# Kernel tuning notes

Hardware: AMD Instinct MI355X
Metric: run time of the kernel (lower is better)

The kernel has to match this reference:

```python
import jax, jax.numpy as jnp
import numpy as np

EPS = 1e-5  # torch LayerNorm default
B, S, D, H = 1, 2048, 512, 32
DH = D // H
DFF = 2 * D


def _ln(x, g, b):
    m = jnp.mean(x, -1, keepdims=True)
    v = jnp.var(x, -1, keepdims=True)
    return (x - m) * jax.lax.rsqrt(v + EPS) * g + b


def setup_inputs() -> dict:
    key = jax.random.key(0)
    ks = iter(jax.random.split(key, 24))
    sc = 1.0 / np.sqrt(D)

    def lin(k, din, dout):  # weight stored [in, out]; y = x @ W + b
        return jax.random.normal(k, (din, dout), jnp.float32) * (1.0 / np.sqrt(din))

    inp = {
        "x": jax.random.normal(next(ks), (B, S, D), jnp.float32),
        # outer pre-norm
        "ln0_g": jnp.ones((D,), jnp.float32), "ln0_b": jnp.zeros((D,), jnp.float32),
        # MultiHead per-branch LayerNorms (3 distinct param sets)
        "lnq_g": jnp.ones((D,), jnp.float32), "lnq_b": jnp.zeros((D,), jnp.float32),
        "lnk_g": jnp.ones((D,), jnp.float32), "lnk_b": jnp.zeros((D,), jnp.float32),
        "lnv_g": jnp.ones((D,), jnp.float32), "lnv_b": jnp.zeros((D,), jnp.float32),
        # QKV + output projections
        "Wq": lin(next(ks), D, D), "bq": jax.random.normal(next(ks), (D,), jnp.float32) * sc,
        "Wk": lin(next(ks), D, D), "bk": jax.random.normal(next(ks), (D,), jnp.float32) * sc,
        "Wv": lin(next(ks), D, D), "bv": jax.random.normal(next(ks), (D,), jnp.float32) * sc,
        "Wo": lin(next(ks), D, D), "bo": jax.random.normal(next(ks), (D,), jnp.float32) * sc,
        # FFN
        "lnf_g": jnp.ones((D,), jnp.float32), "lnf_b": jnp.zeros((D,), jnp.float32),
        "W1": lin(next(ks), D, DFF), "b1": jax.random.normal(next(ks), (DFF,), jnp.float32) * sc,
        "W2": lin(next(ks), DFF, D), "b2": jax.random.normal(next(ks), (D,), jnp.float32) * (1.0 / np.sqrt(DFF)),
    }
    return inp


def reference(x, ln0_g, ln0_b, lnq_g, lnq_b, lnk_g, lnk_b, lnv_g, lnv_b,
              Wq, bq, Wk, bk, Wv, bv, Wo, bo, lnf_g, lnf_b, W1, b1, W2, b2):
    # Encoder: x = norm(x); out = MHA(x,x,x) + x; x = out + FFN(out)
    xn = _ln(x, ln0_g, ln0_b)

    # --- MultiHead (dropout = identity, eval mode) ---
    q = _ln(xn, lnq_g, lnq_b) @ Wq + bq
    k = _ln(xn, lnk_g, lnk_b) @ Wk + bk
    v = _ln(xn, lnv_g, lnv_b) @ Wv + bv
    # [B,S,D] -> [B,H,S,DH]
    q = q.reshape(B, S, H, DH).transpose(0, 2, 1, 3)
    k = k.reshape(B, S, H, DH).transpose(0, 2, 1, 3)
    v = v.reshape(B, S, H, DH).transpose(0, 2, 1, 3)

    scores = jnp.einsum("bhqd,bhkd->bhqk", q, k) / (DH ** 0.5)
    causal = jnp.tril(jnp.ones((S, S), bool))  # make_mask: triu(k=1)==0
    scores = jnp.where(causal, scores, jnp.float32(-1e9))
    attn = jax.nn.softmax(scores, axis=-1)
    ctx = jnp.einsum("bhqk,bhkd->bhqd", attn, v)
    ctx = ctx.transpose(0, 2, 1, 3).reshape(B, S, D)
    mha = ctx @ Wo + bo

    out = mha + xn  # first residual

    # --- FFN branch: LN -> Linear(2D) -> ReLU -> Linear(D) -> ReLU ---
    h = jax.nn.relu(_ln(out, lnf_g, lnf_b) @ W1 + b1)
    ffn = jax.nn.relu(h @ W2 + b2)
    return out + ffn
```

## Files before the change

### kernel.cpp

```cpp
#include <hip/hip_runtime.h>

#define S 2048
#define D 512
#define NH 32
#define DHD 16
#define DFF 1024
#define EPS 1e-5f
#define C1 0.36067376022224085f

typedef unsigned short u16;
typedef __attribute__((ext_vector_type(8))) short short8;
typedef __attribute__((ext_vector_type(4))) float f32x4;
typedef __attribute__((ext_vector_type(16))) float f32x16;
typedef __attribute__((ext_vector_type(4))) unsigned short us4;

#define GL_LDS(gsrc, ldst)                                                   \
  __builtin_amdgcn_global_load_lds(                                          \
      (const __attribute__((address_space(1))) unsigned int*)(gsrc),         \
      (__attribute__((address_space(3))) unsigned int*)(ldst), 16, 0, 0)

static __device__ __forceinline__ u16 f2bf(float f) {
  union { float f; unsigned int i; } c; c.f = f;
  unsigned int x = c.i;
  return (u16)((x + 0x7fffu + ((x >> 16) & 1u)) >> 16);
}
static __device__ __forceinline__ float bf2f(u16 v) {
  union { unsigned int i; float f; } c; c.i = ((unsigned int)v) << 16;
  return c.f;
}

static __device__ __forceinline__ float tmax16(const float* p) {
  float a0 = fmaxf(p[0], p[1]), a1 = fmaxf(p[2], p[3]);
  float a2 = fmaxf(p[4], p[5]), a3 = fmaxf(p[6], p[7]);
  float a4 = fmaxf(p[8], p[9]), a5 = fmaxf(p[10], p[11]);
  float a6 = fmaxf(p[12], p[13]), a7 = fmaxf(p[14], p[15]);
  float b0 = fmaxf(a0, a1), b1 = fmaxf(a2, a3);
  float b2 = fmaxf(a4, a5), b3 = fmaxf(a6, a7);
  return fmaxf(fmaxf(b0, b1), fmaxf(b2, b3));
}
static __device__ __forceinline__ float tsum16(const float* p) {
  float a0 = p[0] + p[1], a1 = p[2] + p[3], a2 = p[4] + p[5], a3 = p[6] + p[7];
  float a4 = p[8] + p[9], a5 = p[10] + p[11], a6 = p[12] + p[13], a7 = p[14] + p[15];
  float b0 = a0 + a1, b1 = a2 + a3, b2 = a4 + a5, b3 = a6 + a7;
  return (b0 + b1) + (b2 + b3);
}

static __device__ __forceinline__ void block_reduce2(float& a, float& b, float* sm, int t) {
#pragma unroll
  for (int m = 1; m <= 32; m <<= 1) {
    a += __shfl_xor(a, m);
    b += __shfl_xor(b, m);
  }
  int w = t >> 6;
  if ((t & 63) == 0) { sm[w] = a; sm[4 + w] = b; }
  __syncthreads();
  a = sm[0] + sm[1] + sm[2] + sm[3];
  b = sm[4] + sm[5] + sm[6] + sm[7];
  __syncthreads();
}

__global__ __launch_bounds__(256) void ln0_kernel(
    const float* __restrict__ x,
    const float* __restrict__ g0, const float* __restrict__ b0,
    const float* __restrict__ gq, const float* __restrict__ bq,
    const float* __restrict__ gk, const float* __restrict__ bk,
    const float* __restrict__ gv, const float* __restrict__ bv,
    float* __restrict__ xn, u16* __restrict__ qin, u16* __restrict__ kin,
    u16* __restrict__ vin) {
  __shared__ float red[8];
  int row = blockIdx.x, t = threadIdx.x;
  const float* xr = x + (size_t)row * D;
  float a0 = xr[t], a1 = xr[t + 256];
  float s = a0 + a1, ss = a0 * a0 + a1 * a1;
  block_reduce2(s, ss, red, t);
  float mean = s * (1.0f / D);
  float var = ss * (1.0f / D) - mean * mean;
  float rs = rsqrtf(var + EPS);
  float y0 = (a0 - mean) * rs * g0[t] + b0[t];
  float y1 = (a1 - mean) * rs * g0[t + 256] + b0[t + 256];
  size_t o = (size_t)row * D + t;
  xn[o] = y0;
  xn[o + 256] = y1;
  float s2 = y0 + y1, ss2 = y0 * y0 + y1 * y1;
  block_reduce2(s2, ss2, red, t);
  float m2 = s2 * (1.0f / D);
  float v2 = ss2 * (1.0f / D) - m2 * m2;
  float rs2 = rsqrtf(v2 + EPS);
  float c0 = (y0 - m2) * rs2, c1 = (y1 - m2) * rs2;
  qin[o] = f2bf(c0 * gq[t] + bq[t]);
  qin[o + 256] = f2bf(c1 * gq[t + 256] + bq[t + 256]);
  kin[o] = f2bf(c0 * gk[t] + bk[t]);
  kin[o + 256] = f2bf(c1 * gk[t + 256] + bk[t + 256]);
  vin[o] = f2bf(c0 * gv[t] + bv[t]);
  vin[o + 256] = f2bf(c1 * gv[t + 256] + bv[t + 256]);
}

__global__ __launch_bounds__(256) void ln2_kernel(
    const float* __restrict__ in, const float* __restrict__ g,
    const float* __restrict__ b, u16* __restrict__ out) {
  __shared__ float red[8];
  int row = blockIdx.x, t = threadIdx.x;
  const float* xr = in + (size_t)row * D;
  float a0 = xr[t], a1 = xr[t + 256];
  float s = a0 + a1, ss = a0 * a0 + a1 * a1;
  block_reduce2(s, ss, red, t);
  float mean = s * (1.0f / D);
  float var = ss * (1.0f / D) - mean * mean;
  float rs = rsqrtf(var + EPS);
  size_t o = (size_t)row * D + t;
  out[o] = f2bf((a0 - mean) * rs * g[t] + b[t]);
  out[o + 256] = f2bf((a1 - mean) * rs * g[t + 256] + b[t + 256]);
}

static __device__ __forceinline__ void transpose_core(const float* __restrict__ W,
                                                      u16* __restrict__ Wt, int K, int N,
                                                      float (*tile)[33]) {
  int n0 = blockIdx.x * 32, k0 = blockIdx.y * 32;
  int tx = threadIdx.x, ty = threadIdx.y;
#pragma unroll
  for (int i = 0; i < 4; ++i)
    tile[ty + 8 * i][tx] = W[(size_t)(k0 + ty + 8 * i) * N + n0 + tx];
  __syncthreads();
#pragma unroll
  for (int i = 0; i < 4; ++i)
    Wt[(size_t)(n0 + ty + 8 * i) * K + k0 + tx] = f2bf(tile[tx][ty + 8 * i]);
}

__global__ void transpose4(const float* __restrict__ W0, const float* __restrict__ W1,
                           const float* __restrict__ W2, const float* __restrict__ W3,
                           u16* __restrict__ T0, u16* __restrict__ T1,
                           u16* __restrict__ T2, u16* __restrict__ T3) {
  __shared__ float tile[32][33];
  int z = blockIdx.z;
  const float* W = z == 0 ? W0 : z == 1 ? W1 : z == 2 ? W2 : W3;
  u16* T = z == 0 ? T0 : z == 1 ? T1 : z == 2 ? T2 : T3;
  transpose_core(W, T, D, D, tile);
}

__global__ void transpose_bf16(const float* __restrict__ W, u16* __restrict__ Wt,
                               int K, int N) {
  __shared__ float tile[32][33];
  transpose_core(W, Wt, K, N, tile);
}

static __device__ __forceinline__ void gemm_stage(
    const u16* __restrict__ A, const u16* __restrict__ Bt, int K,
    int m0, int n0, int kk, u16* As, u16* Bs, int w, int lane) {
  int r8 = lane >> 3;
  int c8 = ((lane & 7) ^ r8) * 8;
#pragma unroll
  for (int j = 0; j < 4; ++j) {
    int chunk = j * 4 + w;
    GL_LDS(A + (size_t)(m0 + chunk * 8 + r8) * K + kk + c8, As + chunk * 512);
  }
#pragma unroll
  for (int j = 0; j < 2; ++j) {
    int chunk = j * 4 + w;
    GL_LDS(Bt + (size_t)(n0 + chunk * 8 + r8) * K + kk + c8, Bs + chunk * 512);
  }
}

static __device__ __forceinline__ void gemm_acc128(
    const u16* __restrict__ A, const u16* __restrict__ Bt, int K, int m0, int n0,
    u16 (*As)[8192], u16 (*Bs)[4096], f32x4 acc[4][2]) {
  int t = threadIdx.x, w = t >> 6, lane = t & 63;
  int wm = w >> 1, wn = w & 1;
  int l16 = lane & 15, g4 = lane >> 4;
  gemm_stage(A, Bt, K, m0, n0, 0, As[0], Bs[0], w, lane);
  __syncthreads();
  int pb = 0;
  for (int kk = 0; kk < K; kk += 64) {
    if (kk + 64 < K)
      gemm_stage(A, Bt, K, m0, n0, kk + 64, As[pb ^ 1], Bs[pb ^ 1], w, lane);
#pragma unroll
    for (int ks = 0; ks < 2; ++ks) {
      short8 af[4], bf[2];
#pragma unroll
      for (int mi = 0; mi < 4; ++mi) {
        int row = wm * 64 + mi * 16 + l16;
        af[mi] = *(const short8*)&As[pb][row * 64 + (((ks * 4 + g4) ^ (l16 & 7)) * 8)];
      }
#pragma unroll
      for (int ni = 0; ni < 2; ++ni) {
        int row = wn * 32 + ni * 16 + l16;
        bf[ni] = *(const short8*)&Bs[pb][row * 64 + (((ks * 4 + g4) ^ (l16 & 7)) * 8)];
      }
#pragma unroll
      for (int mi = 0; mi < 4; ++mi)
#pragma unroll
        for (int ni = 0; ni < 2; ++ni)
          acc[mi][ni] = __builtin_amdgcn_mfma_f32_16x16x32_bf16(
              af[mi], bf[ni], acc[mi][ni], 0, 0, 0);
    }
    __syncthreads();
    pb ^= 1;
  }
}

template <bool RELU, bool RESID, bool OUTBF>
__global__ __launch_bounds__(256) void gemm_kernel(
    const u16* __restrict__ A, const u16* __restrict__ Bt,
    const float* __restrict__ bias, const float* __restrict__ resid,
    float* __restrict__ outf, u16* __restrict__ outb, int N, int K) {
  __shared__ u16 As[2][8192];
  __shared__ u16 Bs[2][4096];
  int m0 = blockIdx.x * 128, n0 = blockIdx.y * 64;
  f32x4 acc[4][2] = {};
  gemm_acc128(A, Bt, K, m0, n0, As, Bs, acc);
  int t = threadIdx.x, w = t >> 6, lane = t & 63;
  int wm = w >> 1, wn = w & 1;
  int l16 = lane & 15, g4 = lane >> 4;
#pragma unroll
  for (int mi = 0; mi < 4; ++mi)
#pragma unroll
    for (int ni = 0; ni < 2; ++ni)
#pragma unroll
      for (int r = 0; r < 4; ++r) {
        int row = m0 + wm * 64 + mi * 16 + g4 * 4 + r;
        int col = n0 + wn * 32 + ni * 16 + l16;
        float v = acc[mi][ni][r] + bias[col];
        if (RELU) v = fmaxf(v, 0.0f);
        if (RESID) v += resid[(size_t)row * N + col];
        if (OUTBF)
          outb[(size_t)row * N + col] = f2bf(v);
        else
          outf[(size_t)row * N + col] = v;
      }
}

__global__ __launch_bounds__(256) void gemm_qkv(
    const u16* __restrict__ a0, const u16* __restrict__ a1, const u16* __restrict__ a2,
    const u16* __restrict__ w0, const u16* __restrict__ w1, const u16* __restrict__ w2,
    const float* __restrict__ c0, const float* __restrict__ c1, const float* __restrict__ c2,
    u16* __restrict__ Qb, u16* __restrict__ KtG, u16* __restrict__ VtG) {
  __shared__ u16 As[2][8192];
  __shared__ u16 Bs[2][4096];
  int z = blockIdx.z;
  const u16* A = z == 0 ? a0 : z == 1 ? a1 : a2;
  const u16* Bt = z == 0 ? w0 : z == 1 ? w1 : w2;
  const float* bias = z == 0 ? c0 : z == 1 ? c1 : c2;
  int m0 = blockIdx.x * 128, n0 = blockIdx.y * 64;
  f32x4 acc[4][2] = {};
  gemm_acc128(A, Bt, D, m0, n0, As, Bs, acc);
  int t = threadIdx.x, w = t >> 6, lane = t & 63;
  int wm = w >> 1, wn = w & 1;
  int l16 = lane & 15, g4 = lane >> 4;
#pragma unroll
  for (int mi = 0; mi < 4; ++mi)
#pragma unroll
    for (int ni = 0; ni < 2; ++ni)
#pragma unroll
      for (int r = 0; r < 4; ++r) {
        int row = m0 + wm * 64 + mi * 16 + g4 * 4 + r;
        int col = n0 + wn * 32 + ni * 16 + l16;
        float v = acc[mi][ni][r] + bias[col];
        if (z == 0) {
          Qb[(size_t)row * D + col] = f2bf(v * C1);
        } else if (z == 1) {
          u16 bf = f2bf(v);
          int h = col >> 4, d = col & 15;
          int I = (((row >> 5) * 2 + (d >> 3)) * 32 + (row & 31)) * 8 + (d & 7);
          KtG[(size_t)h * 32768 + I] = bf;
        } else {
          u16 bf = f2bf(v);
          int h = col >> 4, d = col & 15;
          int I = (((row >> 5) * 4 + ((row >> 3) & 3)) * 16 + d) * 8 + (row & 7);
          VtG[(size_t)h * 32768 + I] = bf;
        }
      }
}

__global__ __launch_bounds__(128) void attn_kernel(const u16* __restrict__ Qb,
                                                   const u16* __restrict__ KtG,
                                                   const u16* __restrict__ VtG,
                                                   u16* __restrict__ ctx,
                                                   u16* __restrict__ part) {
  __shared__ u16 Pl[2][2048];

  const int t = threadIdx.x, w = t >> 6, lane = t & 63;
  const int h = blockIdx.y;
  const int f = 143 - blockIdx.x;
  int g = (int)((sqrtf((float)(1 + 2 * f)) - 1.0f) * 0.5f);
  while (2 * (g + 1) * (g + 2) <= f) ++g;
  while (2 * g * (g + 1) > f) --g;
  const int fg = f - 2 * g * (g + 1);
  const int qt = 4 * g + fg / (g + 1);
  const int c = fg - (fg / (g + 1)) * (g + 1);
  const int t0 = 4 * c;
  const int t1 = (4 * c + 3 < qt) ? 4 * c + 3 : qt;

  const int q0w = qt * 64 + w * 32;
  const int lq = lane & 31, hi = lane >> 5;
  const int l16 = lane & 15, g4 = lane >> 4;

  short8 qf = *(const short8*)(Qb + (size_t)(q0w + lq) * D + h * DHD + hi * 8);
  const u16* kp = KtG + (size_t)h * 32768 + (size_t)t0 * 1024 + hi * 256 + lq * 8;
  const u16* vp = VtG + (size_t)h * 32768 + (size_t)t0 * 1024 + g4 * 128 + l16 * 8;

  f32x4 acc[2] = {};
  float Mrun = -1e30f, Lrun = 0.0f;

  short8 kf0 = *(const short8*)kp;
  short8 kf1 = *(const short8*)(kp + 512);
  short8 vf0 = *(const short8*)vp;
  short8 vf1 = *(const short8*)(vp + 512);

  u16* Pw = &Pl[w][0];
  const int pwr = (lq >> 4) * 1024 + (lq & 15) * 8 + 4 * hi;
  const int prd = g4 * 128 + l16 * 8;

  for (int tt = t0; tt <= t1; ++tt) {
    const int kv0 = tt * 64;
    const bool v1 = (kv0 + 32) <= (q0w + 31);
    f32x16 z = {};
    f32x16 st0 = __builtin_amdgcn_mfma_f32_32x32x16_bf16(kf0, qf, z, 0, 0, 0);
    f32x16 st1 = z;
    if (v1) st1 = __builtin_amdgcn_mfma_f32_32x32x16_bf16(kf1, qf, z, 0, 0, 0);

    short8 nk0, nk1, nv0, nv1;
    const bool more = (tt < t1);
    if (more) {
      kp += 1024; vp += 1024;
      nk0 = *(const short8*)kp;
      nk1 = *(const short8*)(kp + 512);
      nv0 = *(const short8*)vp;
      nv1 = *(const short8*)(vp + 512);
    }

    float p0[16], p1[16];
    const int thr0 = q0w + lq - kv0 - 4 * hi;
    if (kv0 + 31 > q0w) {
#pragma unroll
      for (int r = 0; r < 16; ++r) {
        const int rc = (r & 3) + 8 * (r >> 2);
        p0[r] = (rc > thr0) ? -1e30f : st0[r];
      }
    } else {
#pragma unroll
      for (int r = 0; r < 16; ++r) p0[r] = st0[r];
    }
    if (v1) {
      const int thr1 = thr0 - 32;
      if (kv0 + 63 > q0w) {
#pragma unroll
        for (int r = 0; r < 16; ++r) {
          const int rc = (r & 3) + 8 * (r >> 2);
          p1[r] = (rc > thr1) ? -1e30f : st1[r];
        }
      } else {
#pragma unroll
        for (int r = 0; r < 16; ++r) p1[r] = st1[r];
      }
    }

    float mx = tmax16(p0);
    if (v1) mx = fmaxf(mx, tmax16(p1));
    mx = fmaxf(mx, __shfl_xor(mx, 32));
    float Mnew = fmaxf(Mrun, mx);
    float corr = exp2f(Mrun - Mnew);
#pragma unroll
    for (int r = 0; r < 16; ++r) p0[r] = exp2f(p0[r] - Mnew);
    float sum = tsum16(p0);
    if (v1) {
#pragma unroll
      for (int r = 0; r < 16; ++r) p1[r] = exp2f(p1[r] - Mnew);
      sum += tsum16(p1);
    }
    sum += __shfl_xor(sum, 32);
    Lrun = Lrun * corr + sum;
    Mrun = Mnew;

#pragma unroll
    for (int sq = 0; sq < 2; ++sq)
#pragma unroll
      for (int r = 0; r < 4; ++r) {
        float cc = __shfl(corr, sq * 16 + g4 * 4 + r);
        acc[sq][r] *= cc;
      }

#pragma unroll
    for (int k = 0; k < 4; ++k) {
      unsigned int w0, w1;
      asm("v_cvt_pk_bf16_f32 %0, %1, %2" : "=v"(w0) : "v"(p0[4 * k]), "v"(p0[4 * k + 1]));
      asm("v_cvt_pk_bf16_f32 %0, %1, %2" : "=v"(w1) : "v"(p0[4 * k + 2]), "v"(p0[4 * k + 3]));
      uint2 pv; pv.x = w0; pv.y = w1;
      *(uint2*)&Pw[(pwr + k * 128) ^ (k << 4)] = pv;
    }
    if (v1) {
#pragma unroll
      for (int k = 0; k < 4; ++k) {
        unsigned int w0, w1;
        asm("v_cvt_pk_bf16_f32 %0, %1, %2" : "=v"(w0) : "v"(p1[4 * k]), "v"(p1[4 * k + 1]));
        asm("v_cvt_pk_bf16_f32 %0, %1, %2" : "=v"(w1) : "v"(p1[4 * k + 2]), "v"(p1[4 * k + 3]));
        uint2 pv; pv.x = w0; pv.y = w1;
        *(uint2*)&Pw[(pwr + 512 + k * 128) ^ (k << 4)] = pv;
      }
    }

#pragma unroll
    for (int sx = 0; sx < 2; ++sx) {
      if (sx == 0 || v1) {
        short8 vf = sx ? vf1 : vf0;
#pragma unroll
        for (int sq = 0; sq < 2; ++sq) {
          short8 pf = *(const short8*)&Pw[(sq * 1024 + sx * 512 + prd) ^ (g4 << 4)];
          acc[sq] = __builtin_amdgcn_mfma_f32_16x16x32_bf16(pf, vf, acc[sq], 0, 0, 0);
        }
      }
    }

    if (more) { kf0 = nk0; kf1 = nk1; vf0 = nv0; vf1 = nv1; }
  }

  if (g == 0) {
#pragma unroll
    for (int sq = 0; sq < 2; ++sq)
#pragma unroll
      for (int r = 0; r < 4; ++r) {
        int qlr = sq * 16 + g4 * 4 + r;
        float lv = __shfl(Lrun, qlr);
        ctx[(size_t)(q0w + qlr) * D + h * DHD + l16] = f2bf(acc[sq][r] / lv);
      }
  } else {
    const int pslot = 2 * g * (g + 1) + (qt - 4 * g) * (g + 1) - 4 + c;
    u16* ps = part + ((size_t)(h * 140 + pslot)) * 1280;
#pragma unroll
    for (int sq = 0; sq < 2; ++sq)
#pragma unroll
      for (int r = 0; r < 4; ++r) {
        int qlocal = w * 32 + sq * 16 + g4 * 4 + r;
        ps[qlocal * 20 + 4 + l16] = f2bf(acc[sq][r]);
      }
    if (hi == 0) {
      int ql = w * 32 + lq;
      *(float*)(ps + ql * 20) = Mrun;
      *(float*)(ps + ql * 20 + 2) = Lrun;
    }
  }
}

__global__ __launch_bounds__(64) void attn_merge(const u16* __restrict__ part,
                                                 u16* __restrict__ ctx) {
  int qt = 4 + blockIdx.x, h = blockIdx.y, tq = threadIdx.x;
  int g = qt >> 2, nc = g + 1;
  int base = 2 * g * (g + 1) + (qt - 4 * g) * (g + 1) - 4;
  const u16* bp = part + ((size_t)(h * 140 + base)) * 1280 + tq * 20;
  float M = -1e30f;
  for (int c = 0; c < nc; ++c) M = fmaxf(M, *(const float*)(bp + (size_t)c * 1280));
  float L = 0.0f;
  float o[16];
#pragma unroll
  for (int d = 0; d < 16; ++d) o[d] = 0.0f;
  for (int c = 0; c < nc; ++c) {
    const u16* pr = bp + (size_t)c * 1280;
    float m = *(const float*)pr;
    float l = *(const float*)(pr + 2);
    float sc = exp2f(m - M);
    L += l * sc;
#pragma unroll
    for (int k = 0; k < 4; ++k) {
      us4 ov = *(const us4*)(pr + 4 + 4 * k);
#pragma unroll
      for (int j = 0; j < 4; ++j) o[4 * k + j] += bf2f(ov[j]) * sc;
    }
  }
  float inv = 1.0f / L;
  int q = qt * 64 + tq;
  u16* op = ctx + (size_t)q * D + h * DHD;
#pragma unroll
  for (int k = 0; k < 4; ++k) {
    us4 pk;
#pragma unroll
    for (int j = 0; j < 4; ++j) pk[j] = f2bf(o[4 * k + j] * inv);
    *(us4*)(op + 4 * k) = pk;
  }
}

extern "C" void kernel_launch(void* const* d_in, const int* in_sizes, int n_in,
                              void* d_out, int out_size, void* d_ws, size_t ws_size,
                              hipStream_t stream) {
  const float* x = (const float*)d_in[0];
  const float* ln0_g = (const float*)d_in[1];
  const float* ln0_b = (const float*)d_in[2];
  const float* lnq_g = (const float*)d_in[3];
  const float* lnq_b = (const float*)d_in[4];
  const float* lnk_g = (const float*)d_in[5];
  const float* lnk_b = (const float*)d_in[6];
  const float* lnv_g = (const float*)d_in[7];
  const float* lnv_b = (const float*)d_in[8];
  const float* Wq = (const float*)d_in[9];
  const float* bq = (const float*)d_in[10];
  const float* Wk = (const float*)d_in[11];
  const float* bk = (const float*)d_in[12];
  const float* Wv = (const float*)d_in[13];
  const float* bv = (const float*)d_in[14];
  const float* Wo = (const float*)d_in[15];
  const float* bo = (const float*)d_in[16];
  const float* lnf_g = (const float*)d_in[17];
  const float* lnf_b = (const float*)d_in[18];
  const float* W1 = (const float*)d_in[19];
  const float* b1 = (const float*)d_in[20];
  const float* W2 = (const float*)d_in[21];
  const float* b2 = (const float*)d_in[22];

  char* wsp = (char*)d_ws;
  size_t off = 0;
  auto alloc = [&](size_t bytes) -> void* {
    void* p = wsp + off;
    off += (bytes + 255) & ~(size_t)255;
    return p;
  };
  float* xn = (float*)alloc((size_t)S * D * 4);
  u16* Qb = (u16*)alloc((size_t)S * D * 2);
  u16* ctx = (u16*)alloc((size_t)S * D * 2);
  u16* KtG = (u16*)alloc((size_t)S * D * 2);
  u16* VtG = (u16*)alloc((size_t)S * D * 2);
  u16* WqT = (u16*)alloc((size_t)D * D * 2);
  u16* WkT = (u16*)alloc((size_t)D * D * 2);
  u16* WvT = (u16*)alloc((size_t)D * D * 2);
  u16* WoT = (u16*)alloc((size_t)D * D * 2);
  u16* W1T = (u16*)alloc((size_t)D * DFF * 2);
  u16* W2T = (u16*)alloc((size_t)DFF * D * 2);
  char* regB = (char*)alloc((size_t)15 * 1024 * 1024);
  u16* qin = (u16*)regB;
  u16* kin = (u16*)(regB + (size_t)S * D * 2);
  u16* vin = (u16*)(regB + (size_t)S * D * 4);
  u16* part = (u16*)regB;
  float* outb = (float*)regB;
  u16* lnf = (u16*)(regB + (size_t)S * D * 4);
  u16* hbuf = (u16*)(regB + (size_t)S * D * 6);

  dim3 tb(32, 8);
  transpose4<<<dim3(D / 32, D / 32, 4), tb, 0, stream>>>(Wq, Wk, Wv, Wo, WqT, WkT, WvT, WoT);
  transpose_bf16<<<dim3(DFF / 32, D / 32), tb, 0, stream>>>(W1, W1T, D, DFF);
  transpose_bf16<<<dim3(D / 32, DFF / 32), tb, 0, stream>>>(W2, W2T, DFF, D);

  ln0_kernel<<<S, 256, 0, stream>>>(x, ln0_g, ln0_b, lnq_g, lnq_b, lnk_g, lnk_b,
                                    lnv_g, lnv_b, xn, qin, kin, vin);

  gemm_qkv<<<dim3(S / 128, D / 64, 3), 256, 0, stream>>>(
      qin, kin, vin, WqT, WkT, WvT, bq, bk, bv, Qb, KtG, VtG);

  attn_kernel<<<dim3(144, NH), 128, 0, stream>>>(Qb, KtG, VtG, ctx, part);

  attn_merge<<<dim3(28, NH), 64, 0, stream>>>(part, ctx);

  gemm_kernel<false, true, false><<<dim3(S / 128, D / 64), 256, 0, stream>>>(
      ctx, WoT, bo, xn, outb, nullptr, D, D);

  ln2_kernel<<<S, 256, 0, stream>>>(outb, lnf_g, lnf_b, lnf);

  gemm_kernel<true, false, true><<<dim3(S / 128, DFF / 64), 256, 0, stream>>>(
      lnf, W1T, b1, nullptr, nullptr, hbuf, DFF, D);

  gemm_kernel<true, true, false><<<dim3(S / 128, D / 64), 256, 0, stream>>>(
      hbuf, W2T, b2, outb, (float*)d_out, nullptr, D, DFF);

  (void)in_sizes; (void)n_in; (void)out_size; (void)ws_size;
}
```

Measured before the change: 109.2 us.

## Pre-swizzle weights into MFMA fragments, use 64x64 32x32x16 GEMM tiles, lazy softmax rescale

After: 99.87 us. -8.6%, faster.

```diff
diff --git a/kernel.cpp b/kernel.cpp
--- a/kernel.cpp
+++ b/kernel.cpp
@@ -112,120 +112,116 @@
   out[o + 256] = f2bf((a1 - mean) * rs * g[t + 256] + b[t + 256]);
 }
 
-static __device__ __forceinline__ void transpose_core(const float* __restrict__ W,
-                                                      u16* __restrict__ Wt, int K, int N,
-                                                      float (*tile)[33]) {
-  int n0 = blockIdx.x * 32, k0 = blockIdx.y * 32;
+__global__ void prep_weights(const float* __restrict__ Wq, const float* __restrict__ Wk,
+                             const float* __restrict__ Wv, const float* __restrict__ Wo,
+                             const float* __restrict__ W1, const float* __restrict__ W2,
+                             u16* __restrict__ Fq, u16* __restrict__ Fk,
+                             u16* __restrict__ Fv, u16* __restrict__ Fo,
+                             u16* __restrict__ F1, u16* __restrict__ F2) {
+  __shared__ float tile[32][33];
+  int bz = blockIdx.x;
+  const float* W;
+  u16* F;
+  int K, N, n0, k0;
+  if (bz < 1024) {
+    int wi = bz >> 8, tl = bz & 255;
+    W = wi == 0 ? Wq : wi == 1 ? Wk : wi == 2 ? Wv : Wo;
+    F = wi == 0 ? Fq : wi == 1 ? Fk : wi == 2 ? Fv : Fo;
+    K = 512; N = 512;
+    n0 = (tl & 15) * 32; k0 = (tl >> 4) * 32;
+  } else if (bz < 1536) {
+    int tl = bz - 1024;
+    W = W1; F = F1; K = 512; N = 1024;
+    n0 = (tl & 31) * 32; k0 = (tl >> 5) * 32;
+  } else {
+    int tl = bz - 1536;
+    W = W2; F = F2; K = 1024; N = 512;
+    n0 = (tl & 15) * 32; k0 = (tl >> 4) * 32;
+  }
   int tx = threadIdx.x, ty = threadIdx.y;
 #pragma unroll
   for (int i = 0; i < 4; ++i)
     tile[ty + 8 * i][tx] = W[(size_t)(k0 + ty + 8 * i) * N + n0 + tx];
   __syncthreads();
-#pragma unroll
-  for (int i = 0; i < 4; ++i)
-    Wt[(size_t)(n0 + ty + 8 * i) * K + k0 + tx] = f2bf(tile[tx][ty + 8 * i]);
-}
-
-__global__ void transpose4(const float* __restrict__ W0, const float* __restrict__ W1,
-                           const float* __restrict__ W2, const float* __restrict__ W3,
-                           u16* __restrict__ T0, u16* __restrict__ T1,
-                           u16* __restrict__ T2, u16* __restrict__ T3) {
-  __shared__ float tile[32][33];
-  int z = blockIdx.z;
-  const float* W = z == 0 ? W0 : z == 1 ? W1 : z == 2 ? W2 : W3;
-  u16* T = z == 0 ? T0 : z == 1 ? T1 : z == 2 ? T2 : T3;
-  transpose_core(W, T, D, D, tile);
-}
-
-__global__ void transpose_bf16(const float* __restrict__ W, u16* __restrict__ Wt,
-                               int K, int N) {
-  __shared__ float tile[32][33];
-  transpose_core(W, Wt, K, N, tile);
-}
-
-static __device__ __forceinline__ void gemm_stage(
-    const u16* __restrict__ A, const u16* __restrict__ Bt, int K,
-    int m0, int n0, int kk, u16* As, u16* Bs, int w, int lane) {
-  int r8 = lane >> 3;
-  int c8 = ((lane & 7) ^ r8) * 8;
-#pragma unroll
-  for (int j = 0; j < 4; ++j) {
-    int chunk = j * 4 + w;
-    GL_LDS(A + (size_t)(m0 + chunk * 8 + r8) * K + kk + c8, As + chunk * 512);
-  }
-#pragma unroll
-  for (int j = 0; j < 2; ++j) {
-    int chunk = j * 4 + w;
-    GL_LDS(Bt + (size_t)(n0 + chunk * 8 + r8) * K + kk + c8, Bs + chunk * 512);
-  }
-}
-
-static __device__ __forceinline__ void gemm_acc128(
-    const u16* __restrict__ A, const u16* __restrict__ Bt, int K, int m0, int n0,
-    u16 (*As)[8192], u16 (*Bs)[4096], f32x4 acc[4][2]) {
+  int k = k0 + tx;
+  int kpart = ((k >> 3) & 1) * 32;
+  int kj = k & 7;
+#pragma unroll
+  for (int i = 0; i < 4; ++i) {
+    int n = n0 + ty + 8 * i;
+    size_t I = (size_t)((n >> 5) * (K >> 4) + (k >> 4)) * 512 + ((n & 31) + kpart) * 8 + kj;
+    F[I] = f2bf(tile[tx][ty + 8 * i]);
+  }
+}
+
+static __device__ __forceinline__ void stageA(const u16* __restrict__ A, int K,
+                                              int m0, int kk, u16* As, int t) {
+  int r = t >> 3, sl = t & 7;
+  GL_LDS(A + (size_t)(m0 + r) * K + kk + ((sl ^ (r & 7)) * 8), As + t * 8);
+  int r2 = r + 32;
+  GL_LDS(A + (size_t)(m0 + r2) * K + kk + ((sl ^ (r2 & 7)) * 8), As + (t + 256) * 8);
+}
+
+static __device__ __forceinline__ void gemm64_acc(
+    const u16* __restrict__ A, const u16* __restrict__ Wf, int K, int m0,
+    int n32base, u16 (*As)[4096], f32x16& acc) {
   int t = threadIdx.x, w = t >> 6, lane = t & 63;
   int wm = w >> 1, wn = w & 1;
-  int l16 = lane & 15, g4 = lane >> 4;
-  gemm_stage(A, Bt, K, m0, n0, 0, As[0], Bs[0], w, lane);
+  int l31 = lane & 31, hi5 = lane >> 5;
+  const u16* bp = Wf + (size_t)(n32base + wn) * (K >> 4) * 512 + lane * 8;
+  stageA(A, K, m0, 0, As[0], t);
+  short8 bcur[4], bnxt[4];
+#pragma unroll
+  for (int ks = 0; ks < 4; ++ks) bcur[ks] = *(const short8*)(bp + ks * 512);
   __syncthreads();
   int pb = 0;
+  int arow = wm * 32 + l31;
+  int abase = arow * 64;
   for (int kk = 0; kk < K; kk += 64) {
-    if (kk + 64 < K)
-      gemm_stage(A, Bt, K, m0, n0, kk + 64, As[pb ^ 1], Bs[pb ^ 1], w, lane);
-#pragma unroll
-    for (int ks = 0; ks < 2; ++ks) {
-      short8 af[4], bf[2];
-#pragma unroll
-      for (int mi = 0; mi < 4; ++mi) {
-        int row = wm * 64 + mi * 16 + l16;
-        af[mi] = *(const short8*)&As[pb][row * 64 + (((ks * 4 + g4) ^ (l16 & 7)) * 8)];
-      }
-#pragma unroll
-      for (int ni = 0; ni < 2; ++ni) {
-        int row = wn * 32 + ni * 16 + l16;
-        bf[ni] = *(const short8*)&Bs[pb][row * 64 + (((ks * 4 + g4) ^ (l16 & 7)) * 8)];
-      }
-#pragma unroll
-      for (int mi = 0; mi < 4; ++mi)
-#pragma unroll
-        for (int ni = 0; ni < 2; ++ni)
-          acc[mi][ni] = __builtin_amdgcn_mfma_f32_16x16x32_bf16(
-              af[mi], bf[ni], acc[mi][ni], 0, 0, 0);
+    if (kk + 64 < K) {
+      stageA(A, K, m0, kk + 64, As[pb ^ 1], t);
+      const u16* bp2 = bp + (size_t)(kk + 64) * 32;
+#pragma unroll
+      for (int ks = 0; ks < 4; ++ks) bnxt[ks] = *(const short8*)(bp2 + ks * 512);
+    }
+#pragma unroll
+    for (int ks = 0; ks < 4; ++ks) {
+      int slot = (ks * 2 + hi5) ^ (arow & 7);
+      short8 af = *(const short8*)&As[pb][abase + slot * 8];
+      acc = __builtin_amdgcn_mfma_f32_32x32x16_bf16(af, bcur[ks], acc, 0, 0, 0);
     }
     __syncthreads();
     pb ^= 1;
+#pragma unroll
+    for (int ks = 0; ks < 4; ++ks) bcur[ks] = bnxt[ks];
   }
 }
 
 template <bool RELU, bool RESID, bool OUTBF>
 __global__ __launch_bounds__(256) void gemm_kernel(
-    const u16* __restrict__ A, const u16* __restrict__ Bt,
+    const u16* __restrict__ A, const u16* __restrict__ Wf,
     const float* __restrict__ bias, const float* __restrict__ resid,
     float* __restrict__ outf, u16* __restrict__ outb, int N, int K) {
-  __shared__ u16 As[2][8192];
-  __shared__ u16 Bs[2][4096];
-  int m0 = blockIdx.x * 128, n0 = blockIdx.y * 64;
-  f32x4 acc[4][2] = {};
-  gemm_acc128(A, Bt, K, m0, n0, As, Bs, acc);
+  __shared__ u16 As[2][4096];
+  int m0 = blockIdx.x * 64, n0 = blockIdx.y * 64;
+  f32x16 acc = {};
+  gemm64_acc(A, Wf, K, m0, blockIdx.y * 2, As, acc);
   int t = threadIdx.x, w = t >> 6, lane = t & 63;
   int wm = w >> 1, wn = w & 1;
-  int l16 = lane & 15, g4 = lane >> 4;
-#pragma unroll
-  for (int mi = 0; mi < 4; ++mi)
-#pragma unroll
-    for (int ni = 0; ni < 2; ++ni)
-#pragma unroll
-      for (int r = 0; r < 4; ++r) {
-        int row = m0 + wm * 64 + mi * 16 + g4 * 4 + r;
-        int col = n0 + wn * 32 + ni * 16 + l16;
-        float v = acc[mi][ni][r] + bias[col];
-        if (RELU) v = fmaxf(v, 0.0f);
-        if (RESID) v += resid[(size_t)row * N + col];
-        if (OUTBF)
-          outb[(size_t)row * N + col] = f2bf(v);
-        else
-          outf[(size_t)row * N + col] = v;
-      }
+  int l31 = lane & 31, hi5 = lane >> 5;
+  int col = n0 + wn * 32 + l31;
+  float bv = bias[col];
+#pragma unroll
+  for (int r = 0; r < 16; ++r) {
+    int row = m0 + wm * 32 + (r & 3) + 8 * (r >> 2) + 4 * hi5;
+    float v = acc[r] + bv;
+    if (RELU) v = fmaxf(v, 0.0f);
+    if (RESID) v += resid[(size_t)row * N + col];
+    if (OUTBF)
+      outb[(size_t)row * N + col] = f2bf(v);
+    else
+      outf[(size_t)row * N + col] = v;
+  }
 }
 
 __global__ __launch_bounds__(256) void gemm_qkv(
@@ -233,41 +229,34 @@
     const u16* __restrict__ w0, const u16* __restrict__ w1, const u16* __restrict__ w2,
     const float* __restrict__ c0, const float* __restrict__ c1, const float* __restrict__ c2,
     u16* __restrict__ Qb, u16* __restrict__ KtG, u16* __restrict__ VtG) {
-  __shared__ u16 As[2][8192];
-  __shared__ u16 Bs[2][4096];
+  __shared__ u16 As[2][4096];
   int z = blockIdx.z;
   const u16* A = z == 0 ? a0 : z == 1 ? a1 : a2;
-  const u16* Bt = z == 0 ? w0 : z == 1 ? w1 : w2;
+  const u16* Wf = z == 0 ? w0 : z == 1 ? w1 : w2;
   const float* bias = z == 0 ? c0 : z == 1 ? c1 : c2;
-  int m0 = blockIdx.x * 128, n0 = blockIdx.y * 64;
-  f32x4 acc[4][2] = {};
-  gemm_acc128(A, Bt, D, m0, n0, As, Bs, acc);
+  int m0 = blockIdx.x * 64, n0 = blockIdx.y * 64;
+  f32x16 acc = {};
+  gemm64_acc(A, Wf, D, m0, blockIdx.y * 2, As, acc);
   int t = threadIdx.x, w = t >> 6, lane = t & 63;
   int wm = w >> 1, wn = w & 1;
-  int l16 = lane & 15, g4 = lane >> 4;
-#pragma unroll
-  for (int mi = 0; mi < 4; ++mi)
-#pragma unroll
-    for (int ni = 0; ni < 2; ++ni)
-#pragma unroll
-      for (int r = 0; r < 4; ++r) {
-        int row = m0 + wm * 64 + mi * 16 + g4 * 4 + r;
-        int col = n0 + wn * 32 + ni * 16 + l16;
-        float v = acc[mi][ni][r] + bias[col];
-        if (z == 0) {
-          Qb[(size_t)row * D + col] = f2bf(v * C1);
-        } else if (z == 1) {
-          u16 bf = f2bf(v);
-          int h = col >> 4, d = col & 15;
-          int I = (((row >> 5) * 2 + (d >> 3)) * 32 + (row & 31)) * 8 + (d & 7);
-          KtG[(size_t)h * 32768 + I] = bf;
-        } else {
-          u16 bf = f2bf(v);
-          int h = col >> 4, d = col & 15;
-          int I = (((row >> 5) * 4 + ((row >> 3) & 3)) * 16 + d) * 8 + (row & 7);
-          VtG[(size_t)h * 32768 + I] = bf;
-        }
-      }
+  int l31 = lane & 31, hi5 = lane >> 5;
+  int col = n0 + wn * 32 + l31;
+  float bv = bias[col];
+  int h = col >> 4, d = col & 15;
+#pragma unroll
+  for (int r = 0; r < 16; ++r) {
+    int row = m0 + wm * 32 + (r & 3) + 8 * (r >> 2) + 4 * hi5;
+    float v = acc[r] + bv;
+    if (z == 0) {
+      Qb[(size_t)row * D + col] = f2bf(v * C1);
+    } else if (z == 1) {
+      int I = (((row >> 5) * 2 + (d >> 3)) * 32 + (row & 31)) * 8 + (d & 7);
+      KtG[(size_t)h * 32768 + I] = f2bf(v);
+    } else {
+      int I = (((row >> 5) * 4 + ((row >> 3) & 3)) * 16 + d) * 8 + (row & 7);
+      VtG[(size_t)h * 32768 + I] = f2bf(v);
+    }
+  }
 }
 
 __global__ __launch_bounds__(128) void attn_kernel(const u16* __restrict__ Qb,
@@ -356,27 +345,29 @@
     float mx = tmax16(p0);
     if (v1) mx = fmaxf(mx, tmax16(p1));
     mx = fmaxf(mx, __shfl_xor(mx, 32));
-    float Mnew = fmaxf(Mrun, mx);
-    float corr = exp2f(Mrun - Mnew);
-#pragma unroll
-    for (int r = 0; r < 16; ++r) p0[r] = exp2f(p0[r] - Mnew);
+    if (!__all(mx - Mrun <= 8.0f)) {
+      float Mnew = fmaxf(Mrun, mx);
+      float corr = exp2f(Mrun - Mnew);
+      Lrun *= corr;
+      Mrun = Mnew;
+#pragma unroll
+      for (int sq = 0; sq < 2; ++sq)
+#pragma unroll
+        for (int r = 0; r < 4; ++r) {
+          float cc = __shfl(corr, sq * 16 + g4 * 4 + r);
+          acc[sq][r] *= cc;
+        }
+    }
+#pragma unroll
+    for (int r = 0; r < 16; ++r) p0[r] = exp2f(p0[r] - Mrun);
     float sum = tsum16(p0);
     if (v1) {
 #pragma unroll
-      for (int r = 0; r < 16; ++r) p1[r] = exp2f(p1[r] - Mnew);
+      for (int r = 0; r < 16; ++r) p1[r] = exp2f(p1[r] - Mrun);
       sum += tsum16(p1);
     }
     sum += __shfl_xor(sum, 32);
-    Lrun = Lrun * corr + sum;
-    Mrun = Mnew;
-
-#pragma unroll
-    for (int sq = 0; sq < 2; ++sq)
-#pragma unroll
-      for (int r = 0; r < 4; ++r) {
-        float cc = __shfl(corr, sq * 16 + g4 * 4 + r);
-        acc[sq][r] *= cc;
-      }
+    Lrun += sum;
 
 #pragma unroll
     for (int k = 0; k < 4; ++k) {
@@ -515,12 +506,12 @@
   u16* ctx = (u16*)alloc((size_t)S * D * 2);
   u16* KtG = (u16*)alloc((size_t)S * D * 2);
   u16* VtG = (u16*)alloc((size_t)S * D * 2);
-  u16* WqT = (u16*)alloc((size_t)D * D * 2);
-  u16* WkT = (u16*)alloc((size_t)D * D * 2);
-  u16* WvT = (u16*)alloc((size_t)D * D * 2);
-  u16* WoT = (u16*)alloc((size_t)D * D * 2);
-  u16* W1T = (u16*)alloc((size_t)D * DFF * 2);
-  u16* W2T = (u16*)alloc((size_t)DFF * D * 2);
+  u16* WfQ = (u16*)alloc((size_t)D * D * 2);
+  u16* WfK = (u16*)alloc((size_t)D * D * 2);
+  u16* WfV = (u16*)alloc((size_t)D * D * 2);
+  u16* WfO = (u16*)alloc((size_t)D * D * 2);
+  u16* Wf1 = (u16*)alloc((size_t)D * DFF * 2);
+  u16* Wf2 = (u16*)alloc((size_t)DFF * D * 2);
   char* regB = (char*)alloc((size_t)15 * 1024 * 1024);
   u16* qin = (u16*)regB;
   u16* kin = (u16*)(regB + (size_t)S * D * 2);
@@ -530,31 +521,29 @@
   u16* lnf = (u16*)(regB + (size_t)S * D * 4);
   u16* hbuf = (u16*)(regB + (size_t)S * D * 6);
 
-  dim3 tb(32, 8);
-  transpose4<<<dim3(D / 32, D / 32, 4), tb, 0, stream>>>(Wq, Wk, Wv, Wo, WqT, WkT, WvT, WoT);
-  transpose_bf16<<<dim3(DFF / 32, D / 32), tb, 0, stream>>>(W1, W1T, D, DFF);
-  transpose_bf16<<<dim3(D / 32, DFF / 32), tb, 0, stream>>>(W2, W2T, DFF, D);
+  prep_weights<<<dim3(2048), dim3(32, 8), 0, stream>>>(Wq, Wk, Wv, Wo, W1, W2,
+                                                       WfQ, WfK, WfV, WfO, Wf1, Wf2);
 
   ln0_kernel<<<S, 256, 0, stream>>>(x, ln0_g, ln0_b, lnq_g, lnq_b, lnk_g, lnk_b,
                                     lnv_g, lnv_b, xn, qin, kin, vin);
 
-  gemm_qkv<<<dim3(S / 128, D / 64, 3), 256, 0, stream>>>(
-      qin, kin, vin, WqT, WkT, WvT, bq, bk, bv, Qb, KtG, VtG);
+  gemm_qkv<<<dim3(S / 64, D / 64, 3), 256, 0, stream>>>(
+      qin, kin, vin, WfQ, WfK, WfV, bq, bk, bv, Qb, KtG, VtG);
 
   attn_kernel<<<dim3(144, NH), 128, 0, stream>>>(Qb, KtG, VtG, ctx, part);
 
   attn_merge<<<dim3(28, NH), 64, 0, stream>>>(part, ctx);
 
-  gemm_kernel<false, true, false><<<dim3(S / 128, D / 64), 256, 0, stream>>>(
-      ctx, WoT, bo, xn, outb, nullptr, D, D);
+  gemm_kernel<false, true, false><<<dim3(S / 64, D / 64), 256, 0, stream>>>(
+      ctx, WfO, bo, xn, outb, nullptr, D, D);
 
   ln2_kernel<<<S, 256, 0, stream>>>(outb, lnf_g, lnf_b, lnf);
 
-  gemm_kernel<true, false, true><<<dim3(S / 128, DFF / 64), 256, 0, stream>>>(
-      lnf, W1T, b1, nullptr, nullptr, hbuf, DFF, D);
-
-  gemm_kernel<true, true, false><<<dim3(S / 128, D / 64), 256, 0, stream>>>(
-      hbuf, W2T, b2, outb, (float*)d_out, nullptr, D, DFF);
+  gemm_kernel<true, false, true><<<dim3(S / 64, DFF / 64), 256, 0, stream>>>(
+      lnf, Wf1, b1, nullptr, nullptr, hbuf, DFF, D);
+
+  gemm_kernel<true, true, false><<<dim3(S / 64, D / 64), 256, 0, stream>>>(
+      hbuf, Wf2, b2, outb, (float*)d_out, nullptr, D, DFF);
 
   (void)in_sizes; (void)n_in; (void)out_size; (void)ws_size;
 }
```
